# Kernel optimization log

Measured on AMD Instinct MI355X. Metric: run time of the kernel, lower is better.

The kernel has to match this reference:

```python
import jax, jax.numpy as jnp
import numpy as np

HIDDEN = 1024
HEADS = 16
HEAD_DIM = HIDDEN // HEADS
SCALE = 1.0 / np.sqrt(HEAD_DIM)
B, S = 2, 2048


def setup_inputs() -> dict:
    key = jax.random.key(0)
    ks = jax.random.split(key, 12)
    std = 1.0 / np.sqrt(HIDDEN)
    inp = {
        "x": jax.random.normal(ks[0], (B, S, HIDDEN), jnp.float32),
        "pos_emb": jax.random.normal(ks[1], (B, S, HIDDEN), jnp.float32),
        "mask": jnp.ones((B, S, S), jnp.int32),
        "wq": jax.random.normal(ks[2], (HIDDEN, HIDDEN), jnp.float32) * std,
        "bq": jnp.zeros((HIDDEN,), jnp.float32),
        "wk": jax.random.normal(ks[3], (HIDDEN, HIDDEN), jnp.float32) * std,
        "bk": jnp.zeros((HIDDEN,), jnp.float32),
        "wv": jax.random.normal(ks[4], (HIDDEN, HIDDEN), jnp.float32) * std,
        "bv": jnp.zeros((HIDDEN,), jnp.float32),
        "wo": jax.random.normal(ks[5], (HIDDEN, HIDDEN), jnp.float32) * std,
        "bo": jnp.zeros((HIDDEN,), jnp.float32),
        "w_pos": jax.random.normal(ks[6], (HEADS, HIDDEN), jnp.float32) * std,
    }
    return inp


def reference(x, pos_emb, mask, wq, bq, wk, bk, wv, bv, wo, bo, w_pos):
    b, s, d = x.shape
    # QKV projections (torch Linear: y = x @ W.T + b), split into heads -> (b, h, s, hd)
    q = (x @ wq.T + bq).reshape(b, s, HEADS, HEAD_DIM).transpose(0, 2, 1, 3)
    k = (x @ wk.T + bk).reshape(b, s, HEADS, HEAD_DIM).transpose(0, 2, 1, 3)
    v = (x @ wv.T + bv).reshape(b, s, HEADS, HEAD_DIM).transpose(0, 2, 1, 3)
    # learned positional bias: (b, s, heads) -> (b, heads, s), broadcast over query axis
    pos_bias = (pos_emb @ w_pos.T).transpose(0, 2, 1)  # (b, h, s_key)
    scores = jnp.einsum("bhqd,bhkd->bhqk", q, k) * SCALE
    scores = scores + pos_bias[:, :, None, :]
    scores = jnp.where(mask[:, None, :, :] == 0, -jnp.inf, scores)
    attn = jax.nn.softmax(scores.astype(jnp.float32), axis=-1).astype(q.dtype)
    # dropout p=0.0 -> identity
    out = jnp.einsum("bhqk,bhkd->bhqd", attn, v)
    out = out.transpose(0, 2, 1, 3).reshape(b, s, d)
    return out @ wo.T + bo
```

## Files before the change

### kernel.cpp

```cpp
#include <hip/hip_runtime.h>
#include <stdint.h>

typedef unsigned short u16;
typedef unsigned int u32;
typedef unsigned long long u64;
typedef __attribute__((ext_vector_type(8))) short short8;
typedef __attribute__((ext_vector_type(4))) float f32x4;

#define MFMA16(a,b,c) __builtin_amdgcn_mfma_f32_16x16x32_bf16((a),(b),(c),0,0,0)

__device__ __forceinline__ u16 f2bf(float f){
  u32 u = __builtin_bit_cast(u32, f);
  u32 r = u + 0x7FFFu + ((u >> 16) & 1u);
  return (u16)(r >> 16);
}

__device__ __forceinline__ void gload16(const void* g, void* l){
  __builtin_amdgcn_global_load_lds((__attribute__((address_space(1))) void*)(uintptr_t)g,
                                   (__attribute__((address_space(3))) void*)l, 16, 0, 0);
}

__global__ __launch_bounds__(256) void k_prep(const float* __restrict__ x,
    const float* __restrict__ wq, const float* __restrict__ wk,
    const float* __restrict__ wv, const float* __restrict__ wo,
    u16* __restrict__ xb, u16* __restrict__ wqb, u16* __restrict__ wkb,
    u16* __restrict__ wvb, u16* __restrict__ wob){
  for (int j = blockIdx.x*blockDim.x + threadIdx.x; j < 2097152; j += gridDim.x*blockDim.x){
    const float* src; u16* dst; int off;
    if (j < 1048576){ src = x; dst = xb; off = j; }
    else {
      int r = (j - 1048576) >> 18; off = (j - 1048576) & 262143;
      src = (r==0)?wq:(r==1)?wk:(r==2)?wv:wo;
      dst = (r==0)?wqb:(r==1)?wkb:(r==2)?wvb:wob;
    }
    float4 v = ((const float4*)src)[off];
    ushort4 o;
    o.x = f2bf(v.x); o.y = f2bf(v.y); o.z = f2bf(v.z); o.w = f2bf(v.w);
    ((ushort4*)dst)[off] = o;
  }
}

__global__ __launch_bounds__(256) void k_posb(const float* __restrict__ pos,
    const float* __restrict__ wpos, float* __restrict__ posb){
  int row = blockIdx.x*4 + (threadIdx.x >> 6);
  int lane = threadIdx.x & 63;
  const float* pr = pos + (size_t)row*1024;
  float pv[16];
  #pragma unroll
  for (int t=0;t<4;t++){
    float4 v = ((const float4*)pr)[lane + 64*t];
    pv[4*t+0]=v.x; pv[4*t+1]=v.y; pv[4*t+2]=v.z; pv[4*t+3]=v.w;
  }
  int b = row >> 11, s = row & 2047;
  for (int h=0; h<16; h++){
    const float* wr = wpos + h*1024;
    float acc = 0.f;
    #pragma unroll
    for (int t=0;t<4;t++){
      float4 w = ((const float4*)wr)[lane + 64*t];
      acc += pv[4*t+0]*w.x + pv[4*t+1]*w.y + pv[4*t+2]*w.z + pv[4*t+3]*w.w;
    }
    #pragma unroll
    for (int m=1;m<64;m<<=1) acc += __shfl_xor(acc, m);
    if (lane == 0) posb[(b*16 + h)*2048 + s] = acc * 1.44269504f;
  }
}

__global__ __launch_bounds__(256) void k_mask(const int* __restrict__ mask, u64* __restrict__ pm){
  int wi = (blockIdx.x*blockDim.x + threadIdx.x) >> 6;
  int lane = threadIdx.x & 63;
  int nw = (gridDim.x*blockDim.x) >> 6;
  for (int w = wi; w < 131072; w += nw){
    int v = mask[(size_t)w*64 + lane];
    u64 bits = __ballot(v != 0);
    if (lane == 0) pm[w] = bits;
  }
}

__global__ __launch_bounds__(256) void k_qkv(const u16* __restrict__ xb,
    const u16* __restrict__ wqb, const u16* __restrict__ wkb, const u16* __restrict__ wvb,
    const float* __restrict__ bq, const float* __restrict__ bk, const float* __restrict__ bv,
    u16* __restrict__ Q, u16* __restrict__ K, u16* __restrict__ V){
  __shared__ __align__(16) u16 As[2][128*32];
  __shared__ __align__(16) u16 Bs[2][128*32];
  const int bx = blockIdx.x, by = blockIdx.y;
  const int tid = threadIdx.x, wid = tid >> 6, lane = tid & 63;
  const int wsel = by >> 3;
  const u16* W = (wsel==0) ? wqb : (wsel==1 ? wkb : wvb);
  const float* bias = (wsel==0) ? bq : (wsel==1 ? bk : bv);
  u16* dst = (wsel==0) ? Q : (wsel==1 ? K : V);
  const int m0 = bx*128, n0 = (by & 7)*128;
  const int wm = wid >> 1, wn = wid & 1;
  const int g8 = (lane >> 4)*8;

  auto stage = [&](int kt, int buf){
    #pragma unroll
    for (int jj=0;jj<2;jj++){
      int sp = wid*2 + jj;
      int p = sp*64 + lane;
      int row = p >> 2, c4 = p & 3;
      gload16(xb + (size_t)(m0+row)*1024 + kt*32 + c4*8, &As[buf][sp*512]);
      gload16(W  + (size_t)(n0+row)*1024 + kt*32 + c4*8, &Bs[buf][sp*512]);
    }
  };

  f32x4 acc[4][4];
  f32x4 z4 = {0.f,0.f,0.f,0.f};
  #pragma unroll
  for (int mf=0;mf<4;mf++)
    #pragma unroll
    for (int nf=0;nf<4;nf++) acc[mf][nf] = z4;

  stage(0, 0);
  __syncthreads();
  for (int kt=0; kt<32; kt++){
    int cur = kt & 1;
    if (kt+1 < 32) stage(kt+1, cur^1);
    short8 a[4], b[4];
    #pragma unroll
    for (int mf=0;mf<4;mf++) a[mf] = *(const short8*)&As[cur][(wm*64 + mf*16 + (lane&15))*32 + g8];
    #pragma unroll
    for (int nf=0;nf<4;nf++) b[nf] = *(const short8*)&Bs[cur][(wn*64 + nf*16 + (lane&15))*32 + g8];
    #pragma unroll
    for (int mf=0;mf<4;mf++)
      #pragma unroll
      for (int nf=0;nf<4;nf++) acc[mf][nf] = MFMA16(a[mf], b[nf], acc[mf][nf]);
    __syncthreads();
  }

  #pragma unroll
  for (int nf=0;nf<4;nf++){
    int nloc = n0 + wn*64 + nf*16 + (lane & 15);
    float bb = bias[nloc];
    int h = nloc >> 6, d = nloc & 63;
    #pragma unroll
    for (int mf=0;mf<4;mf++)
      #pragma unroll
      for (int i=0;i<4;i++){
        int m = m0 + wm*64 + mf*16 + (lane>>4)*4 + i;
        int bt = m >> 11, s = m & 2047;
        u16 val = f2bf(acc[mf][nf][i] + bb);
        if (wsel == 2)
          dst[((size_t)((bt*16 + h)*64 + d))*2048 + s] = val;
        else
          dst[((size_t)((bt*16 + h)*2048 + s))*64 + d] = val;
      }
  }
}

__global__ __launch_bounds__(256) void k_attn(const u16* __restrict__ Qg, const u16* __restrict__ Kg,
    const u16* __restrict__ Vtg, const float* __restrict__ posb, const u64* __restrict__ pmask,
    u16* __restrict__ AO){
  __shared__ __align__(16) u16 Ks[2][64*64];
  __shared__ __align__(16) u16 Vts[2][64*64];
  __shared__ __align__(16) u16 Ps[4*16*64];
  const int bid0 = blockIdx.x;
  const int bid = (bid0 & 7)*128 + (bid0 >> 3);
  const int bh = bid >> 5;
  const int qt = bid & 31;
  const int b_ = bh >> 4;
  const int h_ = bh & 15;
  const int tid = threadIdx.x, wid = tid >> 6, lane = tid & 63;
  const int g = lane >> 4, c = lane & 15;
  const int q0w = qt*64 + wid*16;
  const float SC = 0.125f * 1.44269504f;

  short8 qf0, qf1;
  {
    const u16* qp = Qg + ((size_t)(bh*2048 + q0w + c))*64 + g*8;
    qf0 = *(const short8*)qp;
    qf1 = *(const short8*)(qp + 32);
  }
  f32x4 Oa[4];
  f32x4 z4 = {0.f,0.f,0.f,0.f};
  #pragma unroll
  for (int i=0;i<4;i++) Oa[i] = z4;
  float mi[4], li[4];
  #pragma unroll
  for (int i=0;i<4;i++){ mi[i] = -1e30f; li[i] = 0.f; }

  u16* Pw = Ps + wid*1024;

  auto stage = [&](int kt, int buf){
    if (wid < 2){
      #pragma unroll
      for (int jj=0;jj<4;jj++){
        int sx = wid*4 + jj;
        int p = sx*64 + lane;
        int key = p >> 3, o16 = p & 7;
        gload16(Kg + ((size_t)(bh*2048 + kt*64 + key))*64 + (o16 ^ (key&7))*8, &Ks[buf][sx*512]);
      }
    } else {
      #pragma unroll
      for (int jj=0;jj<4;jj++){
        int sv = (wid-2)*4 + jj;
        int p = sv*64 + lane;
        int d = p >> 3, o16 = p & 7;
        gload16(Vtg + ((size_t)(bh*64 + d))*2048 + kt*64 + (o16 ^ (d&7))*8, &Vts[buf][sv*512]);
      }
    }
  };

  stage(0, 0);
  __syncthreads();

  for (int kt=0; kt<32; kt++){
    const int cur = kt & 1;
    if (kt+1 < 32) stage(kt+1, cur^1);

    f32x4 sc[4];
    #pragma unroll
    for (int nf=0;nf<4;nf++) sc[nf] = z4;
    #pragma unroll
    for (int ks=0;ks<2;ks++){
      short8 qf = ks ? qf1 : qf0;
      #pragma unroll
      for (int nf=0;nf<4;nf++){
        int key = nf*16 + c;
        unsigned off = (unsigned)(key*128 + ks*64 + g*16) ^ (unsigned)((key&7)<<4);
        short8 kb = *(const short8*)((const char*)&Ks[cur][0] + off);
        sc[nf] = MFMA16(qf, kb, sc[nf]);
      }
    }

    float pb[4];
    #pragma unroll
    for (int nf=0;nf<4;nf++) pb[nf] = posb[bh*2048 + kt*64 + nf*16 + c];
    u64 mw[4];
    #pragma unroll
    for (int i=0;i<4;i++) mw[i] = pmask[((size_t)(b_*2048 + q0w + g*4 + i))*32 + kt];

    float pv_[4][4], lmax[4];
    #pragma unroll
    for (int i=0;i<4;i++){
      u64 m = mw[i];
      #pragma unroll
      for (int nf=0;nf<4;nf++) pv_[nf][i] = sc[nf][i]*SC + pb[nf];
      if (m != ~0ull){
        #pragma unroll
        for (int nf=0;nf<4;nf++)
          if (!((m >> (nf*16 + c)) & 1ull)) pv_[nf][i] = -1e30f;
      }
      lmax[i] = fmaxf(fmaxf(pv_[0][i], pv_[1][i]), fmaxf(pv_[2][i], pv_[3][i]));
    }
    float need = fmaxf(fmaxf(lmax[0]-mi[0], lmax[1]-mi[1]),
                       fmaxf(lmax[2]-mi[2], lmax[3]-mi[3]));
    if (__any(need > 8.0f)){
      #pragma unroll
      for (int i=0;i<4;i++){
        float t = lmax[i];
        t = fmaxf(t, __shfl_xor(t, 1));
        t = fmaxf(t, __shfl_xor(t, 2));
        t = fmaxf(t, __shfl_xor(t, 4));
        t = fmaxf(t, __shfl_xor(t, 8));
        float mn = fmaxf(mi[i], t);
        float al = __builtin_amdgcn_exp2f(mi[i] - mn);
        mi[i] = mn;
        li[i] *= al;
        #pragma unroll
        for (int db=0;db<4;db++) Oa[db][i] *= al;
      }
    }
    #pragma unroll
    for (int i=0;i<4;i++){
      float rs = 0.f;
      #pragma unroll
      for (int nf=0;nf<4;nf++){
        float e = __builtin_amdgcn_exp2f(pv_[nf][i] - mi[i]);
        pv_[nf][i] = e;
        rs += e;
      }
      li[i] += rs;
    }

    #pragma unroll
    for (int i=0;i<4;i++){
      int qr = g*4 + i;
      #pragma unroll
      for (int nf=0;nf<4;nf++){
        unsigned off = (unsigned)(qr*128 + (nf*16 + c)*2) ^ (unsigned)((qr&7)<<4);
        *(u16*)((char*)Pw + off) = f2bf(pv_[nf][i]);
      }
    }

    #pragma unroll
    for (int ks=0;ks<2;ks++){
      unsigned aoff = (unsigned)(c*128 + ks*64 + g*16) ^ (unsigned)((c&7)<<4);
      short8 pa = *(const short8*)((const char*)Pw + aoff);
      #pragma unroll
      for (int db=0;db<4;db++){
        int d = db*16 + c;
        unsigned boff = (unsigned)(d*128 + ks*64 + g*16) ^ (unsigned)((d&7)<<4);
        short8 vb = *(const short8*)((const char*)&Vts[cur][0] + boff);
        Oa[db] = MFMA16(pa, vb, Oa[db]);
      }
    }
    __syncthreads();
  }

  #pragma unroll
  for (int i=0;i<4;i++){
    float s = li[i];
    s += __shfl_xor(s, 1);
    s += __shfl_xor(s, 2);
    s += __shfl_xor(s, 4);
    s += __shfl_xor(s, 8);
    float inv = 1.0f / s;
    int q = q0w + g*4 + i;
    size_t base = ((size_t)(b_*2048 + q))*1024 + h_*64;
    #pragma unroll
    for (int db=0;db<4;db++)
      AO[base + db*16 + c] = f2bf(Oa[db][i] * inv);
  }
}

__global__ __launch_bounds__(256) void k_out(const u16* __restrict__ A, const u16* __restrict__ W,
    const float* __restrict__ bo, float* __restrict__ out){
  __shared__ __align__(16) u16 As[2][128*32];
  __shared__ __align__(16) u16 Bs[2][128*32];
  const int bx = blockIdx.x, by = blockIdx.y;
  const int tid = threadIdx.x, wid = tid >> 6, lane = tid & 63;
  const int m0 = bx*128, n0 = by*128;
  const int wm = wid >> 1, wn = wid & 1;
  const int g8 = (lane >> 4)*8;

  auto stage = [&](int kt, int buf){
    #pragma unroll
    for (int jj=0;jj<2;jj++){
      int sp = wid*2 + jj;
      int p = sp*64 + lane;
      int row = p >> 2, c4 = p & 3;
      gload16(A + (size_t)(m0+row)*1024 + kt*32 + c4*8, &As[buf][sp*512]);
      gload16(W + (size_t)(n0+row)*1024 + kt*32 + c4*8, &Bs[buf][sp*512]);
    }
  };

  f32x4 acc[4][4];
  f32x4 z4 = {0.f,0.f,0.f,0.f};
  #pragma unroll
  for (int mf=0;mf<4;mf++)
    #pragma unroll
    for (int nf=0;nf<4;nf++) acc[mf][nf] = z4;

  stage(0, 0);
  __syncthreads();
  for (int kt=0; kt<32; kt++){
    int cur = kt & 1;
    if (kt+1 < 32) stage(kt+1, cur^1);
    short8 a[4], b[4];
    #pragma unroll
    for (int mf=0;mf<4;mf++) a[mf] = *(const short8*)&As[cur][(wm*64 + mf*16 + (lane&15))*32 + g8];
    #pragma unroll
    for (int nf=0;nf<4;nf++) b[nf] = *(const short8*)&Bs[cur][(wn*64 + nf*16 + (lane&15))*32 + g8];
    #pragma unroll
    for (int mf=0;mf<4;mf++)
      #pragma unroll
      for (int nf=0;nf<4;nf++) acc[mf][nf] = MFMA16(a[mf], b[nf], acc[mf][nf]);
    __syncthreads();
  }

  #pragma unroll
  for (int nf=0;nf<4;nf++){
    int n = n0 + wn*64 + nf*16 + (lane & 15);
    float bb = bo[n];
    #pragma unroll
    for (int mf=0;mf<4;mf++)
      #pragma unroll
      for (int i=0;i<4;i++){
        int m = m0 + wm*64 + mf*16 + (lane>>4)*4 + i;
        out[(size_t)m*1024 + n] = acc[mf][nf][i] + bb;
      }
  }
}

extern "C" void kernel_launch(void* const* d_in, const int* in_sizes, int n_in,
                              void* d_out, int out_size, void* d_ws, size_t ws_size,
                              hipStream_t stream){
  const float* x    = (const float*)d_in[0];
  const float* pos  = (const float*)d_in[1];
  const int*   mask = (const int*)d_in[2];
  const float* wq   = (const float*)d_in[3];
  const float* bq   = (const float*)d_in[4];
  const float* wk   = (const float*)d_in[5];
  const float* bk   = (const float*)d_in[6];
  const float* wv   = (const float*)d_in[7];
  const float* bv   = (const float*)d_in[8];
  const float* wo   = (const float*)d_in[9];
  const float* bo   = (const float*)d_in[10];
  const float* wpos = (const float*)d_in[11];
  float* out = (float*)d_out;

  char* ws = (char*)d_ws;
  u16* xb   = (u16*)(ws);
  u16* wqb  = (u16*)(ws + ((size_t)8  << 20));
  u16* wkb  = (u16*)(ws + ((size_t)10 << 20));
  u16* wvb  = (u16*)(ws + ((size_t)12 << 20));
  u16* wob  = (u16*)(ws + ((size_t)14 << 20));
  u16* Qb   = (u16*)(ws + ((size_t)16 << 20));
  u16* Kb   = (u16*)(ws + ((size_t)24 << 20));
  u16* Vtb  = (u16*)(ws + ((size_t)32 << 20));
  u16* AO   = (u16*)(ws + ((size_t)40 << 20));
  float* posb = (float*)(ws + ((size_t)48 << 20));
  u64* pm   = (u64*)(ws + ((size_t)49 << 20));

  k_prep<<<dim3(2048), dim3(256), 0, stream>>>(x, wq, wk, wv, wo, xb, wqb, wkb, wvb, wob);
  k_posb<<<dim3(1024), dim3(256), 0, stream>>>(pos, wpos, posb);
  k_mask<<<dim3(1024), dim3(256), 0, stream>>>(mask, pm);
  k_qkv<<<dim3(32,24), dim3(256), 0, stream>>>(xb, wqb, wkb, wvb, bq, bk, bv, Qb, Kb, Vtb);
  k_attn<<<dim3(1024), dim3(256), 0, stream>>>(Qb, Kb, Vtb, posb, pm, AO);
  k_out<<<dim3(32,8), dim3(256), 0, stream>>>(AO, wob, bo, out);
}
```

Measured before the change: 330.3 us.

## Merge prep kernels, permute K rows for packed P stores, add MFMA priority hints

Merges the bf16 conversion, positional-bias and mask-packing kernels into one launch split by block index, which removes two kernel launches and their gaps. In attention, K rows are permuted on load so that each lane owns adjacent keys. That lets the position bias load as float2, the mask bits be tested pairwise, and P be written as packed bf16 pairs with v_cvt_pk_bf16_f32 (32-bit LDS stores instead of 16-bit). s_setprio hints are placed around the MFMA blocks. The permutation has to stay consistent between the score columns and the mask, bias and P layout, otherwise results are wrong. The packed conversion may also round differently from the software f2bf.

Measured after the change: 312.1 us. 5.5% less time.

```diff
diff --git a/kernel.cpp b/kernel.cpp
--- a/kernel.cpp
+++ b/kernel.cpp
@@ -15,6 +15,12 @@
   return (u16)(r >> 16);
 }
 
+__device__ __forceinline__ u32 pk_bf16(float lo, float hi){
+  u32 w;
+  asm("v_cvt_pk_bf16_f32 %0, %1, %2" : "=v"(w) : "v"(lo), "v"(hi));
+  return w;
+}
+
 __device__ __forceinline__ void gload16(const void* g, void* l){
   __builtin_amdgcn_global_load_lds((__attribute__((address_space(1))) void*)(uintptr_t)g,
                                    (__attribute__((address_space(3))) void*)l, 16, 0, 0);
@@ -23,57 +29,58 @@
 __global__ __launch_bounds__(256) void k_prep(const float* __restrict__ x,
     const float* __restrict__ wq, const float* __restrict__ wk,
     const float* __restrict__ wv, const float* __restrict__ wo,
+    const float* __restrict__ pos, const float* __restrict__ wpos,
+    const int* __restrict__ mask,
     u16* __restrict__ xb, u16* __restrict__ wqb, u16* __restrict__ wkb,
-    u16* __restrict__ wvb, u16* __restrict__ wob){
-  for (int j = blockIdx.x*blockDim.x + threadIdx.x; j < 2097152; j += gridDim.x*blockDim.x){
-    const float* src; u16* dst; int off;
-    if (j < 1048576){ src = x; dst = xb; off = j; }
-    else {
-      int r = (j - 1048576) >> 18; off = (j - 1048576) & 262143;
-      src = (r==0)?wq:(r==1)?wk:(r==2)?wv:wo;
-      dst = (r==0)?wqb:(r==1)?wkb:(r==2)?wvb:wob;
-    }
-    float4 v = ((const float4*)src)[off];
-    ushort4 o;
-    o.x = f2bf(v.x); o.y = f2bf(v.y); o.z = f2bf(v.z); o.w = f2bf(v.w);
-    ((ushort4*)dst)[off] = o;
-  }
-}
-
-__global__ __launch_bounds__(256) void k_posb(const float* __restrict__ pos,
-    const float* __restrict__ wpos, float* __restrict__ posb){
-  int row = blockIdx.x*4 + (threadIdx.x >> 6);
-  int lane = threadIdx.x & 63;
-  const float* pr = pos + (size_t)row*1024;
-  float pv[16];
-  #pragma unroll
-  for (int t=0;t<4;t++){
-    float4 v = ((const float4*)pr)[lane + 64*t];
-    pv[4*t+0]=v.x; pv[4*t+1]=v.y; pv[4*t+2]=v.z; pv[4*t+3]=v.w;
-  }
-  int b = row >> 11, s = row & 2047;
-  for (int h=0; h<16; h++){
-    const float* wr = wpos + h*1024;
-    float acc = 0.f;
+    u16* __restrict__ wvb, u16* __restrict__ wob,
+    float* __restrict__ posb, u64* __restrict__ pm){
+  const int bx = blockIdx.x;
+  if (bx < 2048){
+    for (int j = bx*256 + threadIdx.x; j < 2097152; j += 2048*256){
+      const float* src; u16* dst; int off;
+      if (j < 1048576){ src = x; dst = xb; off = j; }
+      else {
+        int r = (j - 1048576) >> 18; off = (j - 1048576) & 262143;
+        src = (r==0)?wq:(r==1)?wk:(r==2)?wv:wo;
+        dst = (r==0)?wqb:(r==1)?wkb:(r==2)?wvb:wob;
+      }
+      float4 v = ((const float4*)src)[off];
+      ushort4 o;
+      o.x = f2bf(v.x); o.y = f2bf(v.y); o.z = f2bf(v.z); o.w = f2bf(v.w);
+      ((ushort4*)dst)[off] = o;
+    }
+  } else if (bx < 3072){
+    int row = (bx - 2048)*4 + (threadIdx.x >> 6);
+    int lane = threadIdx.x & 63;
+    const float* pr = pos + (size_t)row*1024;
+    float pv[16];
     #pragma unroll
     for (int t=0;t<4;t++){
-      float4 w = ((const float4*)wr)[lane + 64*t];
-      acc += pv[4*t+0]*w.x + pv[4*t+1]*w.y + pv[4*t+2]*w.z + pv[4*t+3]*w.w;
-    }
-    #pragma unroll
-    for (int m=1;m<64;m<<=1) acc += __shfl_xor(acc, m);
-    if (lane == 0) posb[(b*16 + h)*2048 + s] = acc * 1.44269504f;
-  }
-}
-
-__global__ __launch_bounds__(256) void k_mask(const int* __restrict__ mask, u64* __restrict__ pm){
-  int wi = (blockIdx.x*blockDim.x + threadIdx.x) >> 6;
-  int lane = threadIdx.x & 63;
-  int nw = (gridDim.x*blockDim.x) >> 6;
-  for (int w = wi; w < 131072; w += nw){
-    int v = mask[(size_t)w*64 + lane];
-    u64 bits = __ballot(v != 0);
-    if (lane == 0) pm[w] = bits;
+      float4 v = ((const float4*)pr)[lane + 64*t];
+      pv[4*t+0]=v.x; pv[4*t+1]=v.y; pv[4*t+2]=v.z; pv[4*t+3]=v.w;
+    }
+    int b = row >> 11, s = row & 2047;
+    for (int h=0; h<16; h++){
+      const float* wr = wpos + h*1024;
+      float acc = 0.f;
+      #pragma unroll
+      for (int t=0;t<4;t++){
+        float4 w = ((const float4*)wr)[lane + 64*t];
+        acc += pv[4*t+0]*w.x + pv[4*t+1]*w.y + pv[4*t+2]*w.z + pv[4*t+3]*w.w;
+      }
+      #pragma unroll
+      for (int m=1;m<64;m<<=1) acc += __shfl_xor(acc, m);
+      if (lane == 0) posb[(b*16 + h)*2048 + s] = acc * 1.44269504f;
+    }
+  } else {
+    int lb = bx - 3072;
+    int wi = (lb*256 + threadIdx.x) >> 6;
+    int lane = threadIdx.x & 63;
+    for (int w = wi; w < 131072; w += (1024*256)>>6){
+      int v = mask[(size_t)w*64 + lane];
+      u64 bits = __ballot(v != 0);
+      if (lane == 0) pm[w] = bits;
+    }
   }
 }
 
@@ -187,8 +194,9 @@
       for (int jj=0;jj<4;jj++){
         int sx = wid*4 + jj;
         int p = sx*64 + lane;
-        int key = p >> 3, o16 = p & 7;
-        gload16(Kg + ((size_t)(bh*2048 + kt*64 + key))*64 + (o16 ^ (key&7))*8, &Ks[buf][sx*512]);
+        int r = p >> 3, o16 = p & 7;
+        int tau = 2*(r&15) + ((r>>4)&1) + (r&32);
+        gload16(Kg + ((size_t)(bh*2048 + kt*64 + tau))*64 + (o16 ^ (r&7))*8, &Ks[buf][sx*512]);
       }
     } else {
       #pragma unroll
@@ -211,21 +219,22 @@
     f32x4 sc[4];
     #pragma unroll
     for (int nf=0;nf<4;nf++) sc[nf] = z4;
+    __builtin_amdgcn_s_setprio(1);
     #pragma unroll
     for (int ks=0;ks<2;ks++){
       short8 qf = ks ? qf1 : qf0;
       #pragma unroll
       for (int nf=0;nf<4;nf++){
-        int key = nf*16 + c;
-        unsigned off = (unsigned)(key*128 + ks*64 + g*16) ^ (unsigned)((key&7)<<4);
+        int r = nf*16 + c;
+        unsigned off = (unsigned)(r*128 + ks*64 + g*16) ^ (unsigned)((r&7)<<4);
         short8 kb = *(const short8*)((const char*)&Ks[cur][0] + off);
         sc[nf] = MFMA16(qf, kb, sc[nf]);
       }
     }
-
-    float pb[4];
-    #pragma unroll
-    for (int nf=0;nf<4;nf++) pb[nf] = posb[bh*2048 + kt*64 + nf*16 + c];
+    __builtin_amdgcn_s_setprio(0);
+
+    float2 pb01 = *(const float2*)&posb[bh*2048 + kt*64 + 2*c];
+    float2 pb23 = *(const float2*)&posb[bh*2048 + kt*64 + 32 + 2*c];
     u64 mw[4];
     #pragma unroll
     for (int i=0;i<4;i++) mw[i] = pmask[((size_t)(b_*2048 + q0w + g*4 + i))*32 + kt];
@@ -233,13 +242,18 @@
     float pv_[4][4], lmax[4];
     #pragma unroll
     for (int i=0;i<4;i++){
+      pv_[0][i] = sc[0][i]*SC + pb01.x;
+      pv_[1][i] = sc[1][i]*SC + pb01.y;
+      pv_[2][i] = sc[2][i]*SC + pb23.x;
+      pv_[3][i] = sc[3][i]*SC + pb23.y;
       u64 m = mw[i];
-      #pragma unroll
-      for (int nf=0;nf<4;nf++) pv_[nf][i] = sc[nf][i]*SC + pb[nf];
       if (m != ~0ull){
-        #pragma unroll
-        for (int nf=0;nf<4;nf++)
-          if (!((m >> (nf*16 + c)) & 1ull)) pv_[nf][i] = -1e30f;
+        u32 lo = (u32)(m >> (2*c));
+        u32 hi = (u32)(m >> (2*c + 32));
+        if (!(lo & 1u)) pv_[0][i] = -1e30f;
+        if (!(lo & 2u)) pv_[1][i] = -1e30f;
+        if (!(hi & 1u)) pv_[2][i] = -1e30f;
+        if (!(hi & 2u)) pv_[3][i] = -1e30f;
       }
       lmax[i] = fmaxf(fmaxf(pv_[0][i], pv_[1][i]), fmaxf(pv_[2][i], pv_[3][i]));
     }
@@ -276,13 +290,15 @@
     #pragma unroll
     for (int i=0;i<4;i++){
       int qr = g*4 + i;
-      #pragma unroll
-      for (int nf=0;nf<4;nf++){
-        unsigned off = (unsigned)(qr*128 + (nf*16 + c)*2) ^ (unsigned)((qr&7)<<4);
-        *(u16*)((char*)Pw + off) = f2bf(pv_[nf][i]);
-      }
-    }
-
+      u32 w0 = pk_bf16(pv_[0][i], pv_[1][i]);
+      u32 w1 = pk_bf16(pv_[2][i], pv_[3][i]);
+      unsigned o0 = (unsigned)(qr*128 + 4*c) ^ (unsigned)((qr&7)<<4);
+      unsigned o1 = (unsigned)(qr*128 + 64 + 4*c) ^ (unsigned)((qr&7)<<4);
+      *(u32*)((char*)Pw + o0) = w0;
+      *(u32*)((char*)Pw + o1) = w1;
+    }
+
+    __builtin_amdgcn_s_setprio(1);
     #pragma unroll
     for (int ks=0;ks<2;ks++){
       unsigned aoff = (unsigned)(c*128 + ks*64 + g*16) ^ (unsigned)((c&7)<<4);
@@ -295,6 +311,7 @@
         Oa[db] = MFMA16(pa, vb, Oa[db]);
       }
     }
+    __builtin_amdgcn_s_setprio(0);
     __syncthreads();
   }
 
@@ -403,9 +420,8 @@
   float* posb = (float*)(ws + ((size_t)48 << 20));
   u64* pm   = (u64*)(ws + ((size_t)49 << 20));
 
-  k_prep<<<dim3(2048), dim3(256), 0, stream>>>(x, wq, wk, wv, wo, xb, wqb, wkb, wvb, wob);
-  k_posb<<<dim3(1024), dim3(256), 0, stream>>>(pos, wpos, posb);
-  k_mask<<<dim3(1024), dim3(256), 0, stream>>>(mask, pm);
+  k_prep<<<dim3(4096), dim3(256), 0, stream>>>(x, wq, wk, wv, wo, pos, wpos, mask,
+                                               xb, wqb, wkb, wvb, wob, posb, pm);
   k_qkv<<<dim3(32,24), dim3(256), 0, stream>>>(xb, wqb, wkb, wvb, bq, bk, bv, Qb, Kb, Vtb);
   k_attn<<<dim3(1024), dim3(256), 0, stream>>>(Qb, Kb, Vtb, posb, pm, AO);
   k_out<<<dim3(32,8), dim3(256), 0, stream>>>(AO, wob, bo, out);
```
